# Optimization experiments

Measured on AMD Instinct MI355X. Metric: run time of the kernel, lower is better.

Reference implementation:

```python
import jax, jax.numpy as jnp
import numpy as np

D_MODEL = 1024
N_HEADS = 16
D_V = D_MODEL // N_HEADS  # 64


def setup_inputs() -> dict:
    key = jax.random.key(0)
    k1, k2, k3, k4, k5, k6 = jax.random.split(key, 6)
    N, L = 2, 2048
    return {
        "queries": jax.random.normal(k1, (N, L, D_MODEL), jnp.float32),
        "keys": jax.random.normal(k2, (N, L, D_MODEL), jnp.float32),
        "values": jax.random.normal(k3, (N, L, D_MODEL), jnp.float32),
        # key-padding mask, 0 = masked out (broadcast over heads and queries)
        "mask": jax.random.randint(k4, (N, 1, 1, L), 0, 2).astype(jnp.int32),
        # torch nn.Linear(d_model, d_model): weight [out, in], bias [out]
        "fc_w": jax.random.normal(k5, (D_MODEL, D_MODEL), jnp.float32) / np.sqrt(D_MODEL).astype(np.float32),
        "fc_b": jax.random.normal(k6, (D_MODEL,), jnp.float32) * 0.01,
    }


def reference(queries, keys, values, mask, fc_w, fc_b):
    N, Lq, _ = queries.shape
    Lk = keys.shape[1]
    # NOTE: the source defines Q/K/V Linear layers but never applies them in forward.
    q = queries.reshape(N, Lq, N_HEADS, D_V).transpose(0, 2, 1, 3)  # [N,H,Lq,Dv]
    k = keys.reshape(N, Lk, N_HEADS, D_V)                            # [N,Lk,H,Dv]
    v = values.reshape(N, Lk, N_HEADS, D_V)                          # [N,Lk,H,Dv]
    energy = jnp.einsum('nhqd,nkhd->nhqk', q, k)                     # QK^T
    energy = jnp.where(mask == 0, -jnp.inf, energy)                  # masked_fill
    # faithful to source: scale by sqrt(d_model), applied after masking
    attn = jax.nn.softmax(energy / jnp.sqrt(jnp.float32(D_MODEL)), axis=-1)
    out = jnp.einsum('nhqk,nkhd->nqhd', attn, v).reshape(N, Lq, N_HEADS * D_V)
    return out @ fc_w.T + fc_b
```

## Files before the change

### kernel.cpp

```cpp
#include <hip/hip_runtime.h>
#include <hip/hip_bf16.h>

#define SEQL 2048
#define DMODEL 1024

typedef short bf16x8 __attribute__((ext_vector_type(8)));
typedef short bf16x4 __attribute__((ext_vector_type(4)));
typedef float f32x4 __attribute__((ext_vector_type(4)));
typedef unsigned short u16;

__device__ __forceinline__ u16 f2bf(float f) {
    union { float f; unsigned u; } v; v.f = f;
    unsigned r = v.u + 0x7FFFu + ((v.u >> 16) & 1u);
    return (u16)(r >> 16);
}

__device__ __forceinline__ float fexp2(float x) {
#if __has_builtin(__builtin_amdgcn_exp2f)
    return __builtin_amdgcn_exp2f(x);
#else
    return exp2f(x);
#endif
}

#define SCALE2 0.04508422f

__device__ __forceinline__ void async16(u16* lds, const u16* g) {
    __builtin_amdgcn_global_load_lds(
        (const __attribute__((address_space(1))) unsigned int*)g,
        (__attribute__((address_space(3))) unsigned int*)lds,
        16, 0, 0);
}


#define TSTR 72

__global__ __launch_bounds__(256) void pack_all(
    const float* __restrict__ kg, const float* __restrict__ wg,
    const float* __restrict__ vg, const int* __restrict__ mg,
    u16* __restrict__ kb, u16* __restrict__ wb, u16* __restrict__ vtb,
    float* __restrict__ maskf)
{
    __shared__ __align__(16) u16 T[64 * TSTR];
    const int b = blockIdx.x, t = threadIdx.x;
    u16 o[8];
    if (b < 2048) {
        const int e0 = (b * 256 + t) * 8;
        const int n = e0 >> 21;
        const int s = (e0 >> 10) & 2047;
        const int dm = e0 & 1023, h = dm >> 6, d0 = dm & 63;
        const float4 x0 = *(const float4*)(kg + e0);
        const float4 x1 = *(const float4*)(kg + e0 + 4);
        o[0]=f2bf(x0.x); o[1]=f2bf(x0.y); o[2]=f2bf(x0.z); o[3]=f2bf(x0.w);
        o[4]=f2bf(x1.x); o[5]=f2bf(x1.y); o[6]=f2bf(x1.z); o[7]=f2bf(x1.w);
        const int kt = s >> 6, st = (s >> 4) & 3, m = s & 15;
        const int f = d0 >> 5, qd = (d0 >> 3) & 3;
        u16* dst = kb + ((size_t)((n * 16 + h) * 32 + kt)) * 4096
                      + (st * 2 + f) * 512 + (m + 16 * qd) * 8;
        *(bf16x8*)dst = *(bf16x8*)o;
    } else if (b < 2560) {
        const int e0 = ((b - 2048) * 256 + t) * 8;
        const int col = e0 >> 10, k0 = e0 & 1023;
        const float4 x0 = *(const float4*)(wg + e0);
        const float4 x1 = *(const float4*)(wg + e0 + 4);
        o[0]=f2bf(x0.x); o[1]=f2bf(x0.y); o[2]=f2bf(x0.z); o[3]=f2bf(x0.w);
        o[4]=f2bf(x1.x); o[5]=f2bf(x1.y); o[6]=f2bf(x1.z); o[7]=f2bf(x1.w);
        const int cb = col >> 6, cj = (col >> 4) & 3, m = col & 15;
        const int kt = k0 >> 6, f = (k0 >> 5) & 1, qd = (k0 >> 3) & 3;
        u16* dst = wb + ((size_t)((cb * 16 + kt) * 8 + cj * 2 + f)) * 512
                      + (m + 16 * qd) * 8;
        *(bf16x8*)dst = *(bf16x8*)o;
    } else if (b < 3584) {
        const int bb = b - 2560;
        const int kt = bb & 31, h = (bb >> 5) & 15, n = bb >> 9;
        {
            const int s = t >> 2, d0 = (t & 3) * 16;
            const float* src = vg + ((size_t)(n * SEQL + kt * 64 + s) * DMODEL) + h * 64 + d0;
            u16 w16[16];
            #pragma unroll
            for (int j = 0; j < 16; ++j) w16[j] = f2bf(src[j]);
            *(bf16x8*)&T[s * TSTR + d0]     = *(bf16x8*)&w16[0];
            *(bf16x8*)&T[s * TSTR + d0 + 8] = *(bf16x8*)&w16[8];
        }
        __syncthreads();
        {
            const int d = t >> 2, k0 = (t & 3) * 16;
            u16 w16[16];
            #pragma unroll
            for (int j = 0; j < 16; ++j) w16[j] = T[(k0 + j) * TSTR + d];
            const int t4 = d >> 4, dr = d & 15;
            u16* base = vtb + ((size_t)((n * 16 + h) * 32 + kt)) * 4096;
            #pragma unroll
            for (int g = 0; g < 2; ++g) {
                const int key0 = k0 + g * 8;
                const int kk = key0 >> 5, qk = (key0 >> 3) & 3;
                *(bf16x8*)(base + (t4 * 2 + kk) * 512 + (dr + 16 * qk) * 8)
                    = *(bf16x8*)&w16[g * 8];
            }
        }
    } else {
        #pragma unroll
        for (int i = 0; i < 16; ++i) {
            const int idx = t * 16 + i;
            maskf[idx] = mg[idx] ? 0.0f : -1.0e5f;
        }
    }
}

__global__ __launch_bounds__(512) void attn_fused(
    const float* __restrict__ qg, const u16* __restrict__ kb,
    const u16* __restrict__ vtb, const float* __restrict__ maskf,
    u16* __restrict__ xb)
{
    __shared__ __align__(16) u16 SM[32768];

    const int blk = blockIdx.x;
    const int qblk = blk & 15;
    const int h = (blk >> 4) & 15;
    const int n = blk >> 8;
    const int tid = threadIdx.x;
    const int wave = tid >> 6, lane = tid & 63;
    const int half = wave >> 2, w4 = wave & 3;
    const int tloc = tid & 255;
    const int lrow = lane & 15, quad = lane >> 4;
    const int q0 = qblk * 128;

    u16* const K_lds = SM + half * 4096;
    u16* const V_lds = SM + 8192 + half * 4096;
    u16* const P_lds = SM + 16384 + wave * 2048;

    const u16* ksrc = kb  + ((size_t)(n * 16 + h)) * 131072 + (size_t)half * 65536;
    const u16* vsrc = vtb + ((size_t)(n * 16 + h)) * 131072 + (size_t)half * 65536;
    const float* mrow = maskf + n * SEQL + half * 1024;

    bf16x8 qf[2][2];
    #pragma unroll
    for (int qi = 0; qi < 2; ++qi) {
        const float* qp = qg + ((size_t)(n * SEQL + q0 + w4 * 32 + qi * 16 + lrow) * DMODEL) + h * 64 + quad * 8;
        #pragma unroll
        for (int f = 0; f < 2; ++f) {
            const float4 a = *(const float4*)(qp + f * 32);
            const float4 c = *(const float4*)(qp + f * 32 + 4);
            u16* dst = (u16*)&qf[qi][f];
            dst[0]=f2bf(a.x); dst[1]=f2bf(a.y); dst[2]=f2bf(a.z); dst[3]=f2bf(a.w);
            dst[4]=f2bf(c.x); dst[5]=f2bf(c.y); dst[6]=f2bf(c.z); dst[7]=f2bf(c.w);
        }
    }

    bf16x8 onesf;
    #pragma unroll
    for (int j = 0; j < 8; ++j) ((u16*)&onesf)[j] = 0x3F80;

    f32x4 oacc[2][4];
    f32x4 lacc[2];
    #pragma unroll
    for (int qi = 0; qi < 2; ++qi) {
        lacc[qi] = (f32x4){0.f, 0.f, 0.f, 0.f};
        #pragma unroll
        for (int t4 = 0; t4 < 4; ++t4) oacc[qi][t4] = (f32x4){0.f, 0.f, 0.f, 0.f};
    }

    for (int i = 0; i < 16; ++i) {
        __syncthreads();
        {
            const u16* ks = ksrc + (size_t)i * 4096;
            const u16* vs = vsrc + (size_t)i * 4096;
            #pragma unroll
            for (int c = 0; c < 2; ++c) {
                const int ch = tloc + c * 256;
                async16(&K_lds[ch * 8], ks + ch * 8);
                async16(&V_lds[ch * 8], vs + ch * 8);
            }
        }
        __syncthreads();

        #pragma unroll
        for (int st = 0; st < 4; ++st) {
            const bf16x8 kf0 = *(const bf16x8*)&K_lds[(st * 2 + 0) * 512 + lane * 8];
            const bf16x8 kf1 = *(const bf16x8*)&K_lds[(st * 2 + 1) * 512 + lane * 8];
            const f32x4 mv = *(const f32x4*)&mrow[i * 64 + st * 16 + quad * 4];
            const int kk = st >> 1;
            const int qk = (st & 1) * 2 + (quad >> 1);
            const int j0 = (quad & 1) * 4;
            #pragma unroll
            for (int qi = 0; qi < 2; ++qi) {
                f32x4 sa = (f32x4){0.f, 0.f, 0.f, 0.f};
                sa = __builtin_amdgcn_mfma_f32_16x16x32_bf16(kf0, qf[qi][0], sa, 0, 0, 0);
                sa = __builtin_amdgcn_mfma_f32_16x16x32_bf16(kf1, qf[qi][1], sa, 0, 0, 0);
                float e0v = fexp2(fmaf(sa[0], SCALE2, mv[0]));
                float e1v = fexp2(fmaf(sa[1], SCALE2, mv[1]));
                float e2v = fexp2(fmaf(sa[2], SCALE2, mv[2]));
                float e3v = fexp2(fmaf(sa[3], SCALE2, mv[3]));
                __hip_bfloat162 h0 = __float22bfloat162_rn(make_float2(e0v, e1v));
                __hip_bfloat162 h1 = __float22bfloat162_rn(make_float2(e2v, e3v));
                union { unsigned u[2]; bf16x4 v; } pk;
                pk.u[0] = *(unsigned*)&h0;
                pk.u[1] = *(unsigned*)&h1;
                *(bf16x4*)&P_lds[(qi * 2 + kk) * 512 + (lrow + 16 * qk) * 8 + j0] = pk.v;
            }
        }
        asm volatile("s_waitcnt lgkmcnt(0)" ::: "memory");

        bf16x8 vf[4][2];
        #pragma unroll
        for (int t4 = 0; t4 < 4; ++t4) {
            vf[t4][0] = *(const bf16x8*)&V_lds[(t4 * 2 + 0) * 512 + lane * 8];
            vf[t4][1] = *(const bf16x8*)&V_lds[(t4 * 2 + 1) * 512 + lane * 8];
        }
        #pragma unroll
        for (int qi = 0; qi < 2; ++qi) {
            const bf16x8 pf0 = *(const bf16x8*)&P_lds[(qi * 2 + 0) * 512 + lane * 8];
            const bf16x8 pf1 = *(const bf16x8*)&P_lds[(qi * 2 + 1) * 512 + lane * 8];
            lacc[qi] = __builtin_amdgcn_mfma_f32_16x16x32_bf16(pf0, onesf, lacc[qi], 0, 0, 0);
            lacc[qi] = __builtin_amdgcn_mfma_f32_16x16x32_bf16(pf1, onesf, lacc[qi], 0, 0, 0);
            #pragma unroll
            for (int t4 = 0; t4 < 4; ++t4) {
                oacc[qi][t4] = __builtin_amdgcn_mfma_f32_16x16x32_bf16(pf0, vf[t4][0], oacc[qi][t4], 0, 0, 0);
                oacc[qi][t4] = __builtin_amdgcn_mfma_f32_16x16x32_bf16(pf1, vf[t4][1], oacc[qi][t4], 0, 0, 0);
            }
        }
    }

    __syncthreads();
    float* const Pf = (float*)(SM + 16384);
    float* const Lf = (float*)SM;
    if (half) {
        float* dst = Pf + (size_t)(w4 * 64 + lane) * 32;
        float* ld  = Lf + (size_t)(w4 * 64 + lane) * 8;
        #pragma unroll
        for (int qi = 0; qi < 2; ++qi) {
            *(f32x4*)(ld + qi * 4) = lacc[qi];
            #pragma unroll
            for (int t4 = 0; t4 < 4; ++t4)
                *(f32x4*)(dst + qi * 16 + t4 * 4) = oacc[qi][t4];
        }
    }
    __syncthreads();
    if (!half) {
        const float* src = Pf + (size_t)(w4 * 64 + lane) * 32;
        const float* ls  = Lf + (size_t)(w4 * 64 + lane) * 8;
        #pragma unroll
        for (int qi = 0; qi < 2; ++qi) {
            lacc[qi] += *(const f32x4*)(ls + qi * 4);
            #pragma unroll
            for (int t4 = 0; t4 < 4; ++t4)
                oacc[qi][t4] += *(const f32x4*)(src + qi * 16 + t4 * 4);
        }
        #pragma unroll
        for (int qi = 0; qi < 2; ++qi)
            #pragma unroll
            for (int r = 0; r < 4; ++r) {
                const float rinv = 1.0f / lacc[qi][r];
                const int row = n * SEQL + q0 + w4 * 32 + qi * 16 + quad * 4 + r;
                const int rb = row >> 7, rt = (row >> 4) & 7, m = row & 15;
                #pragma unroll
                for (int t4 = 0; t4 < 4; ++t4) {
                    const int f = t4 >> 1;
                    const int qd = (t4 & 1) * 2 + (lrow >> 3);
                    xb[((size_t)((rb * 16 + h) * 16 + rt * 2 + f)) * 512
                       + (m + 16 * qd) * 8 + (lrow & 7)] = f2bf(oacc[qi][t4][r] * rinv);
                }
            }
    }
}

__global__ __launch_bounds__(256) void fc_kernel(
    const u16* __restrict__ xb, const u16* __restrict__ wb,
    const float* __restrict__ bias, float* __restrict__ out)
{
    __shared__ __align__(16) u16 SM[24576];
    u16* const X_lds = SM;
    u16* const W_lds = SM + 16384;

    const int blk = blockIdx.x;
    const int cb = blk & 15, rb = blk >> 4;
    const int tid = threadIdx.x;
    const int wave = tid >> 6, lane = tid & 63;
    const int lrow = lane & 15, quad = lane >> 4;

    const u16* xs0 = xb + ((size_t)rb * 16) * 8192;
    const u16* ws0 = wb + ((size_t)cb * 16) * 4096;

    f32x4 acc[2][4];
    #pragma unroll
    for (int ri = 0; ri < 2; ++ri)
        #pragma unroll
        for (int cj = 0; cj < 4; ++cj) acc[ri][cj] = (f32x4){0.f, 0.f, 0.f, 0.f};

    {
        #pragma unroll
        for (int i = 0; i < 4; ++i) {
            const int ch = tid + i * 256;
            async16(&X_lds[ch * 8], xs0 + ch * 8);
        }
        #pragma unroll
        for (int i = 0; i < 2; ++i) {
            const int ch = tid + i * 256;
            async16(&W_lds[ch * 8], ws0 + ch * 8);
        }
    }
    __syncthreads();

    for (int kt = 0; kt < 16; ++kt) {
        const int cur = kt & 1;
        const u16* const Xc = X_lds + cur * 8192;
        const u16* const Wc = W_lds + cur * 4096;

        if (kt + 1 < 16) {
            const int nxt = cur ^ 1;
            const u16* xs = xs0 + (size_t)(kt + 1) * 8192;
            const u16* ws = ws0 + (size_t)(kt + 1) * 4096;
            #pragma unroll
            for (int i = 0; i < 4; ++i) {
                const int ch = tid + i * 256;
                async16(&X_lds[nxt * 8192 + ch * 8], xs + ch * 8);
            }
            #pragma unroll
            for (int i = 0; i < 2; ++i) {
                const int ch = tid + i * 256;
                async16(&W_lds[nxt * 4096 + ch * 8], ws + ch * 8);
            }
        }

        bf16x8 af[2][2];
        #pragma unroll
        for (int ri = 0; ri < 2; ++ri) {
            af[ri][0] = *(const bf16x8*)&Xc[((wave * 2 + ri) * 2 + 0) * 512 + lane * 8];
            af[ri][1] = *(const bf16x8*)&Xc[((wave * 2 + ri) * 2 + 1) * 512 + lane * 8];
        }
        #pragma unroll
        for (int cj = 0; cj < 4; ++cj) {
            const bf16x8 bf0 = *(const bf16x8*)&Wc[(cj * 2 + 0) * 512 + lane * 8];
            const bf16x8 bf1 = *(const bf16x8*)&Wc[(cj * 2 + 1) * 512 + lane * 8];
            #pragma unroll
            for (int ri = 0; ri < 2; ++ri) {
                acc[ri][cj] = __builtin_amdgcn_mfma_f32_16x16x32_bf16(af[ri][0], bf0, acc[ri][cj], 0, 0, 0);
                acc[ri][cj] = __builtin_amdgcn_mfma_f32_16x16x32_bf16(af[ri][1], bf1, acc[ri][cj], 0, 0, 0);
            }
        }

        __syncthreads();
    }

    const int row0 = rb * 128, col0 = cb * 64;
    #pragma unroll
    for (int ri = 0; ri < 2; ++ri)
        #pragma unroll
        for (int cj = 0; cj < 4; ++cj) {
            const int col = col0 + cj * 16 + lrow;
            const float bv = bias[col];
            #pragma unroll
            for (int r = 0; r < 4; ++r)
                out[(size_t)(row0 + wave * 32 + ri * 16 + quad * 4 + r) * DMODEL + col] = acc[ri][cj][r] + bv;
        }
}

extern "C" void kernel_launch(void* const* d_in, const int* in_sizes, int n_in,
                              void* d_out, int out_size, void* d_ws, size_t ws_size,
                              hipStream_t stream) {
    const float* q   = (const float*)d_in[0];
    const float* k   = (const float*)d_in[1];
    const float* v   = (const float*)d_in[2];
    const int*   m   = (const int*)d_in[3];
    const float* fcw = (const float*)d_in[4];
    const float* fcb = (const float*)d_in[5];
    float* out = (float*)d_out;

    char* ws = (char*)d_ws;
    u16*   kbuf  = (u16*)(ws);
    u16*   vtbuf = (u16*)(ws + (8u  << 20));
    u16*   wbuf  = (u16*)(ws + (16u << 20));
    u16*   xbuf  = (u16*)(ws + (18u << 20));
    float* maskf = (float*)(ws + (26u << 20));

    pack_all<<<dim3(3585), dim3(256), 0, stream>>>(k, fcw, v, m, kbuf, wbuf, vtbuf, maskf);
    attn_fused<<<dim3(512), dim3(512), 0, stream>>>(q, kbuf, vtbuf, maskf, xbuf);
    fc_kernel<<<dim3(512), dim3(256), 0, stream>>>(xbuf, wbuf, fcb, out);
}
```

Baseline: 171.4 us.

## Load K/V fragments directly into registers and remap blocks per XCD

Drops the LDS staging of K and V tiles and the two per-iteration block barriers. Each wave now loads its K and V MFMA fragments straight from global memory into registers, which shrinks shared memory and adds a launch-bounds occupancy hint of 4 blocks. Block indices are also remapped so the 16 query blocks of each (batch, head) land on the same XCD, aiming for better L2 reuse of K/V. The trade-off is that the four waves of each half now fetch the same K/V data redundantly from global or cache, and register pressure rises.

```diff
diff --git a/kernel.cpp b/kernel.cpp
--- a/kernel.cpp
+++ b/kernel.cpp
@@ -107,27 +107,28 @@
     }
 }
 
-__global__ __launch_bounds__(512) void attn_fused(
+__global__ __launch_bounds__(512, 4) void attn_fused(
     const float* __restrict__ qg, const u16* __restrict__ kb,
     const u16* __restrict__ vtb, const float* __restrict__ maskf,
     u16* __restrict__ xb)
 {
-    __shared__ __align__(16) u16 SM[32768];
-
-    const int blk = blockIdx.x;
-    const int qblk = blk & 15;
-    const int h = (blk >> 4) & 15;
-    const int n = blk >> 8;
+    __shared__ __align__(16) u16 SM[20480];
+
+    const int b = blockIdx.x;
+    const int xcd = b & 7;
+    const int j = b >> 3;
+    const int qblk = j & 15;
+    const int hn = xcd * 4 + (j >> 4);
+    const int h = hn & 15;
+    const int n = hn >> 4;
+
     const int tid = threadIdx.x;
     const int wave = tid >> 6, lane = tid & 63;
     const int half = wave >> 2, w4 = wave & 3;
-    const int tloc = tid & 255;
     const int lrow = lane & 15, quad = lane >> 4;
     const int q0 = qblk * 128;
 
-    u16* const K_lds = SM + half * 4096;
-    u16* const V_lds = SM + 8192 + half * 4096;
-    u16* const P_lds = SM + 16384 + wave * 2048;
+    u16* const P_lds = SM + wave * 2048;
 
     const u16* ksrc = kb  + ((size_t)(n * 16 + h)) * 131072 + (size_t)half * 65536;
     const u16* vsrc = vtb + ((size_t)(n * 16 + h)) * 131072 + (size_t)half * 65536;
@@ -149,7 +150,7 @@
 
     bf16x8 onesf;
     #pragma unroll
-    for (int j = 0; j < 8; ++j) ((u16*)&onesf)[j] = 0x3F80;
+    for (int jj = 0; jj < 8; ++jj) ((u16*)&onesf)[jj] = 0x3F80;
 
     f32x4 oacc[2][4];
     f32x4 lacc[2];
@@ -161,23 +162,16 @@
     }
 
     for (int i = 0; i < 16; ++i) {
-        __syncthreads();
-        {
-            const u16* ks = ksrc + (size_t)i * 4096;
-            const u16* vs = vsrc + (size_t)i * 4096;
-            #pragma unroll
-            for (int c = 0; c < 2; ++c) {
-                const int ch = tloc + c * 256;
-                async16(&K_lds[ch * 8], ks + ch * 8);
-                async16(&V_lds[ch * 8], vs + ch * 8);
-            }
-        }
-        __syncthreads();
+        const u16* kp = ksrc + (size_t)i * 4096 + lane * 8;
+        const u16* vp = vsrc + (size_t)i * 4096 + lane * 8;
+        bf16x8 kf[8], vf[8];
+        #pragma unroll
+        for (int f = 0; f < 8; ++f) kf[f] = *(const bf16x8*)(kp + f * 512);
+        #pragma unroll
+        for (int f = 0; f < 8; ++f) vf[f] = *(const bf16x8*)(vp + f * 512);
 
         #pragma unroll
         for (int st = 0; st < 4; ++st) {
-            const bf16x8 kf0 = *(const bf16x8*)&K_lds[(st * 2 + 0) * 512 + lane * 8];
-            const bf16x8 kf1 = *(const bf16x8*)&K_lds[(st * 2 + 1) * 512 + lane * 8];
             const f32x4 mv = *(const f32x4*)&mrow[i * 64 + st * 16 + quad * 4];
             const int kk = st >> 1;
             const int qk = (st & 1) * 2 + (quad >> 1);
@@ -185,8 +179,8 @@
             #pragma unroll
             for (int qi = 0; qi < 2; ++qi) {
                 f32x4 sa = (f32x4){0.f, 0.f, 0.f, 0.f};
-                sa = __builtin_amdgcn_mfma_f32_16x16x32_bf16(kf0, qf[qi][0], sa, 0, 0, 0);
-                sa = __builtin_amdgcn_mfma_f32_16x16x32_bf16(kf1, qf[qi][1], sa, 0, 0, 0);
+                sa = __builtin_amdgcn_mfma_f32_16x16x32_bf16(kf[st * 2 + 0], qf[qi][0], sa, 0, 0, 0);
+                sa = __builtin_amdgcn_mfma_f32_16x16x32_bf16(kf[st * 2 + 1], qf[qi][1], sa, 0, 0, 0);
                 float e0v = fexp2(fmaf(sa[0], SCALE2, mv[0]));
                 float e1v = fexp2(fmaf(sa[1], SCALE2, mv[1]));
                 float e2v = fexp2(fmaf(sa[2], SCALE2, mv[2]));
@@ -201,12 +195,6 @@
         }
         asm volatile("s_waitcnt lgkmcnt(0)" ::: "memory");
 
-        bf16x8 vf[4][2];
-        #pragma unroll
-        for (int t4 = 0; t4 < 4; ++t4) {
-            vf[t4][0] = *(const bf16x8*)&V_lds[(t4 * 2 + 0) * 512 + lane * 8];
-            vf[t4][1] = *(const bf16x8*)&V_lds[(t4 * 2 + 1) * 512 + lane * 8];
-        }
         #pragma unroll
         for (int qi = 0; qi < 2; ++qi) {
             const bf16x8 pf0 = *(const bf16x8*)&P_lds[(qi * 2 + 0) * 512 + lane * 8];
@@ -215,15 +203,15 @@
             lacc[qi] = __builtin_amdgcn_mfma_f32_16x16x32_bf16(pf1, onesf, lacc[qi], 0, 0, 0);
             #pragma unroll
             for (int t4 = 0; t4 < 4; ++t4) {
-                oacc[qi][t4] = __builtin_amdgcn_mfma_f32_16x16x32_bf16(pf0, vf[t4][0], oacc[qi][t4], 0, 0, 0);
-                oacc[qi][t4] = __builtin_amdgcn_mfma_f32_16x16x32_bf16(pf1, vf[t4][1], oacc[qi][t4], 0, 0, 0);
+                oacc[qi][t4] = __builtin_amdgcn_mfma_f32_16x16x32_bf16(pf0, vf[t4 * 2 + 0], oacc[qi][t4], 0, 0, 0);
+                oacc[qi][t4] = __builtin_amdgcn_mfma_f32_16x16x32_bf16(pf1, vf[t4 * 2 + 1], oacc[qi][t4], 0, 0, 0);
             }
         }
     }
 
     __syncthreads();
-    float* const Pf = (float*)(SM + 16384);
-    float* const Lf = (float*)SM;
+    float* const Pf = (float*)SM;
+    float* const Lf = (float*)(SM + 16384);
     if (half) {
         float* dst = Pf + (size_t)(w4 * 64 + lane) * 32;
         float* ld  = Lf + (size_t)(w4 * 64 + lane) * 8;
```

Result: no change. 173.5 us (+1.2%).
